# Kernel optimization log

Measured on AMD Instinct MI355X. Metric: run time of the kernel, lower is better.

The kernel has to match this reference:

```python
import jax, jax.numpy as jnp
import numpy as np

N = 50000      # nodes
E = 800000     # edges (before self-loops)
IN_C = 128
H_C = 64
HEADS = 4
OUT_C = 16
NEG_SLOPE = 0.2  # PyG GATConv default


def setup_inputs() -> dict:
    key = jax.random.key(0)
    ks = jax.random.split(key, 11)
    x = jax.random.normal(ks[0], (N, IN_C), dtype=jnp.float32)
    edge_index = jax.random.randint(ks[1], (2, E), 0, N, dtype=jnp.int64)
    def p(k, shape, fan_in):
        return jax.random.normal(k, shape, dtype=jnp.float32) / np.sqrt(fan_in)
    return {
        "x": x,
        "edge_index": edge_index,
        "W1": p(ks[2], (IN_C, HEADS * H_C), IN_C),
        "att_src1": p(ks[3], (HEADS, H_C), H_C),
        "att_dst1": p(ks[4], (HEADS, H_C), H_C),
        "b1": jnp.zeros((HEADS * H_C,), dtype=jnp.float32),
        "W2": p(ks[5], (HEADS * H_C, OUT_C), HEADS * H_C),
        "att_src2": p(ks[6], (1, OUT_C), OUT_C),
        "att_dst2": p(ks[7], (1, OUT_C), OUT_C),
        "b2": jnp.zeros((OUT_C,), dtype=jnp.float32),
    }


def _gat_layer(x, src, dst, W, a_src, a_dst, b, concat):
    n = x.shape[0]
    heads, C = a_src.shape
    h = (x @ W).reshape(n, heads, C)                      # [N,H,C]
    al_s = jnp.einsum('nhc,hc->nh', h, a_src)             # [N,H]
    al_d = jnp.einsum('nhc,hc->nh', h, a_dst)
    e = jax.nn.leaky_relu(al_s[src] + al_d[dst], NEG_SLOPE)  # [E,H]
    # segment softmax over destination neighborhoods
    m = jax.lax.stop_gradient(jax.ops.segment_max(e, dst, num_segments=n))
    p = jnp.exp(e - m[dst])
    denom = jax.ops.segment_sum(p, dst, num_segments=n)
    alpha = p / (denom[dst] + 1e-16)                      # [E,H]
    out = jax.ops.segment_sum(alpha[:, :, None] * h[src], dst, num_segments=n)  # [N,H,C]
    out = out.reshape(n, heads * C) if concat else out.mean(axis=1)
    return out + b


def reference(x, edge_index, W1, att_src1, att_dst1, b1, W2, att_src2, att_dst2, b2):
    # PyG GATConv add_self_loops=True
    loop = jnp.arange(N, dtype=edge_index.dtype)
    src = jnp.concatenate([edge_index[0], loop])
    dst = jnp.concatenate([edge_index[1], loop])
    h = jax.nn.relu(_gat_layer(x, src, dst, W1, att_src1, att_dst1, b1, True))
    out = _gat_layer(h, src, dst, W2, att_src2, att_dst2, b2, False)
    return jax.nn.log_softmax(out, axis=-1)
```

## Files before the change

### kernel.cpp

```cpp
#include <hip/hip_runtime.h>
#include <hip/hip_fp16.h>
#include <cstdint>
#include <cstddef>

#define NEG 0.2f

typedef _Float16 f16x8 __attribute__((ext_vector_type(8)));
typedef float f32x4 __attribute__((ext_vector_type(4)));

__device__ inline float lrelu(float v) { return v > 0.f ? v : NEG * v; }

__global__ void k_swzW(const float* __restrict__ W1, f16x8* __restrict__ W1s) {
  int tau = blockIdx.x * 256 + threadIdx.x;
  if (tau >= 4096) return;
  int l = tau & 63, ct = (tau >> 6) & 15, ks = tau >> 10;
  int col = ct * 16 + (l & 15);
  f16x8 v;
  #pragma unroll
  for (int j = 0; j < 8; j++) {
    int k = ks * 32 + ((j < 4) ? ((l >> 4) * 4 + j) : (16 + (l >> 4) * 4 + (j - 4)));
    v[j] = (_Float16)W1[k * 256 + col];
  }
  W1s[tau] = v;
}

__global__ __launch_bounds__(256) void k_gemm1f(const float* __restrict__ X,
                                                const f16x8* __restrict__ W1s,
                                                const float* __restrict__ as1,
                                                const float* __restrict__ ad1,
                                                __half* __restrict__ H16,
                                                float* __restrict__ als,
                                                float* __restrict__ ald, int N) {
  __shared__ __align__(16) char lds[32768];
  _Float16* A = (_Float16*)lds;
  int t = threadIdx.x;
  int rb = blockIdx.x * 64;
  int l = t & 63, wv = t >> 6;

  #pragma unroll
  for (int i = 0; i < 8; i++) {
    int idx = i * 256 + t;
    int row = idx >> 5, q = idx & 31;
    int gr = rb + row; if (gr >= N) gr = N - 1;
    float4 xv = *(const float4*)(X + (size_t)gr * 128 + q * 4);
    int ks = q >> 3, g = q & 3, hg = (q >> 2) & 1;
    int gran = (ks * 4 + g) ^ (row & 7);
    _Float16* dst = A + row * 128 + gran * 8 + hg * 4;
    dst[0] = (_Float16)xv.x; dst[1] = (_Float16)xv.y;
    dst[2] = (_Float16)xv.z; dst[3] = (_Float16)xv.w;
  }
  __syncthreads();

  f32x4 acc[4][4] = {};
  #pragma unroll
  for (int ks = 0; ks < 4; ks++) {
    f16x8 bfr[4];
    #pragma unroll
    for (int ct = 0; ct < 4; ct++)
      bfr[ct] = W1s[(ks * 16 + wv * 4 + ct) * 64 + l];
    #pragma unroll
    for (int rt = 0; rt < 4; rt++) {
      int row = rt * 16 + (l & 15);
      int gran = (ks * 4 + (l >> 4)) ^ (row & 7);
      f16x8 afr = *(const f16x8*)(A + row * 128 + gran * 8);
      #pragma unroll
      for (int ct = 0; ct < 4; ct++)
        acc[rt][ct] = __builtin_amdgcn_mfma_f32_16x16x32_f16(afr, bfr[ct], acc[rt][ct], 0, 0, 0);
    }
  }

  float asv[4], adv[4];
  #pragma unroll
  for (int ct = 0; ct < 4; ct++) {
    asv[ct] = as1[wv * 64 + ct * 16 + (l & 15)];
    adv[ct] = ad1[wv * 64 + ct * 16 + (l & 15)];
  }
  #pragma unroll
  for (int rt = 0; rt < 4; rt++) {
    #pragma unroll
    for (int j = 0; j < 4; j++) {
      float ps = 0.f, pd = 0.f;
      #pragma unroll
      for (int ct = 0; ct < 4; ct++) {
        ps += acc[rt][ct][j] * asv[ct];
        pd += acc[rt][ct][j] * adv[ct];
      }
      ps += __shfl_xor(ps, 1); ps += __shfl_xor(ps, 2);
      ps += __shfl_xor(ps, 4); ps += __shfl_xor(ps, 8);
      pd += __shfl_xor(pd, 1); pd += __shfl_xor(pd, 2);
      pd += __shfl_xor(pd, 4); pd += __shfl_xor(pd, 8);
      if ((l & 15) == 0) {
        int gr = rb + rt * 16 + (l >> 4) * 4 + j;
        if (gr < N) { als[gr * 4 + wv] = ps; ald[gr * 4 + wv] = pd; }
      }
    }
  }

  __syncthreads();
  _Float16* HL = (_Float16*)lds;
  #pragma unroll
  for (int rt = 0; rt < 4; rt++) {
    #pragma unroll
    for (int j = 0; j < 4; j++) {
      int row = rt * 16 + (l >> 4) * 4 + j;
      #pragma unroll
      for (int ct = 0; ct < 4; ct++) {
        int col = wv * 64 + ct * 16 + (l & 15);
        int g2 = (col >> 3) ^ ((row & 7) << 2);
        HL[row * 256 + g2 * 8 + (col & 7)] = (_Float16)acc[rt][ct][j];
      }
    }
  }
  __syncthreads();
  #pragma unroll
  for (int i = 0; i < 8; i++) {
    int idx = i * 256 + t;
    int row = idx >> 5, g = idx & 31;
    int g2 = g ^ ((row & 7) << 2);
    f32x4 v = *(const f32x4*)(HL + row * 256 + g2 * 8);
    int gr = rb + row;
    if (gr < N) *(f32x4*)((char*)H16 + (size_t)gr * 512 + g * 16) = v;
  }
}

__global__ void k_deg(const int* __restrict__ ei, int* __restrict__ deg, int E, int ET) {
  int e = blockIdx.x * 256 + threadIdx.x;
  if (e >= ET) return;
  int d = (e < E) ? ei[E + e] : e - E;
  atomicAdd(&deg[d], 1);
}

__global__ __launch_bounds__(256) void k_scan_partial(const int* __restrict__ deg,
                                                      int* __restrict__ bsum, int N) {
  __shared__ int sd[256];
  int t = threadIdx.x;
  int base = blockIdx.x * 1024 + t * 4;
  int s = 0;
  #pragma unroll
  for (int j = 0; j < 4; j++) { int i = base + j; s += (i < N) ? deg[i] : 0; }
  sd[t] = s;
  __syncthreads();
  for (int o = 128; o > 0; o >>= 1) {
    if (t < o) sd[t] += sd[t + o];
    __syncthreads();
  }
  if (t == 0) bsum[blockIdx.x] = sd[0];
}

__global__ void k_scan_sums(const int* __restrict__ bsum, int* __restrict__ boff,
                            int* __restrict__ offsets, int NB, int N) {
  if (threadIdx.x == 0 && blockIdx.x == 0) {
    int run = 0;
    for (int i = 0; i < NB; i++) { boff[i] = run; run += bsum[i]; }
    offsets[N] = run;
  }
}

__global__ __launch_bounds__(256) void k_scan_final(const int* __restrict__ deg,
                                                    const int* __restrict__ boff,
                                                    int* __restrict__ offsets,
                                                    int* __restrict__ cursor, int N) {
  __shared__ int sd[256];
  int t = threadIdx.x;
  int base = blockIdx.x * 1024 + t * 4;
  int v[4]; int s = 0;
  #pragma unroll
  for (int j = 0; j < 4; j++) { int i = base + j; v[j] = (i < N) ? deg[i] : 0; s += v[j]; }
  int my = s;
  sd[t] = s;
  __syncthreads();
  for (int o = 1; o < 256; o <<= 1) {
    int add = (t >= o) ? sd[t - o] : 0;
    __syncthreads();
    sd[t] += add;
    __syncthreads();
  }
  int run = sd[t] - my + boff[blockIdx.x];
  #pragma unroll
  for (int j = 0; j < 4; j++) {
    int i = base + j;
    if (i < N) { offsets[i] = run; cursor[i] = run; run += v[j]; }
  }
}

__global__ void k_fill(const int* __restrict__ ei, int* __restrict__ cursor,
                       int* __restrict__ csr_src, int E, int ET) {
  int e = blockIdx.x * 256 + threadIdx.x;
  if (e >= ET) return;
  int s, d;
  if (e < E) { s = ei[e]; d = ei[E + e]; } else { s = d = e - E; }
  int pos = atomicAdd(&cursor[d], 1);
  csr_src[pos] = s;
}

__device__ inline void acc8(float4 v, float p, float* a, float& s) {
  __half2 h0 = __builtin_bit_cast(__half2, v.x);
  __half2 h1 = __builtin_bit_cast(__half2, v.y);
  __half2 h2 = __builtin_bit_cast(__half2, v.z);
  __half2 h3 = __builtin_bit_cast(__half2, v.w);
  float2 f0 = __half22float2(h0), f1 = __half22float2(h1);
  float2 f2 = __half22float2(h2), f3 = __half22float2(h3);
  a[0] += p * f0.x; a[1] += p * f0.y; a[2] += p * f1.x; a[3] += p * f1.y;
  a[4] += p * f2.x; a[5] += p * f2.y; a[6] += p * f3.x; a[7] += p * f3.y;
  s += p;
}

__global__ __launch_bounds__(256) void k_agg1(const int* __restrict__ off,
                                              const int* __restrict__ csr_src,
                                              const float* __restrict__ als1,
                                              const float* __restrict__ ald1,
                                              const float4* __restrict__ H16,
                                              const float* __restrict__ b1,
                                              __half* __restrict__ H2, int N) {
  int t = threadIdx.x;
  int n = blockIdx.x * 8 + (t >> 5);
  if (n >= N) return;
  int lane = t & 31;
  int g = lane >> 3;
  float aldn = ald1[n * 4 + g];
  int st = off[n], en = off[n + 1];
  float a[8] = {0.f, 0.f, 0.f, 0.f, 0.f, 0.f, 0.f, 0.f};
  float s = 0.f;
  int i = st;
  for (; i + 4 <= en; i += 4) {
    int s0 = csr_src[i], s1 = csr_src[i + 1], s2 = csr_src[i + 2], s3 = csr_src[i + 3];
    float p0 = __expf(lrelu(als1[s0 * 4 + g] + aldn));
    float p1 = __expf(lrelu(als1[s1 * 4 + g] + aldn));
    float p2 = __expf(lrelu(als1[s2 * 4 + g] + aldn));
    float p3 = __expf(lrelu(als1[s3 * 4 + g] + aldn));
    float4 v0 = H16[(size_t)s0 * 32 + lane];
    float4 v1 = H16[(size_t)s1 * 32 + lane];
    float4 v2 = H16[(size_t)s2 * 32 + lane];
    float4 v3 = H16[(size_t)s3 * 32 + lane];
    acc8(v0, p0, a, s); acc8(v1, p1, a, s); acc8(v2, p2, a, s); acc8(v3, p3, a, s);
  }
  for (; i < en; i++) {
    int s0 = csr_src[i];
    float p0 = __expf(lrelu(als1[s0 * 4 + g] + aldn));
    float4 v0 = H16[(size_t)s0 * 32 + lane];
    acc8(v0, p0, a, s);
  }
  float inv = 1.f / (s + 1e-16f);
  int c0 = lane * 8;
  float4 bb0 = *(const float4*)(b1 + c0);
  float4 bb1 = *(const float4*)(b1 + c0 + 4);
  f16x8 o;
  o[0] = (_Float16)fmaxf(a[0] * inv + bb0.x, 0.f);
  o[1] = (_Float16)fmaxf(a[1] * inv + bb0.y, 0.f);
  o[2] = (_Float16)fmaxf(a[2] * inv + bb0.z, 0.f);
  o[3] = (_Float16)fmaxf(a[3] * inv + bb0.w, 0.f);
  o[4] = (_Float16)fmaxf(a[4] * inv + bb1.x, 0.f);
  o[5] = (_Float16)fmaxf(a[5] * inv + bb1.y, 0.f);
  o[6] = (_Float16)fmaxf(a[6] * inv + bb1.z, 0.f);
  o[7] = (_Float16)fmaxf(a[7] * inv + bb1.w, 0.f);
  *(f16x8*)((char*)H2 + (size_t)n * 512 + lane * 16) = o;
}

__global__ __launch_bounds__(256) void k_gemm2(const __half* __restrict__ H2,
                                               const float* __restrict__ W2,
                                               const float* __restrict__ as2,
                                               const float* __restrict__ ad2,
                                               float* __restrict__ Z,
                                               float* __restrict__ als2,
                                               float* __restrict__ ald2, int N) {
  __shared__ float w2s[4096];
  int t = threadIdx.x;
  for (int i = t; i < 4096; i += 256) w2s[i] = W2[i];
  __syncthreads();
  int n = blockIdx.x * 16 + (t >> 4);
  int c = t & 15;
  if (n >= N) return;
  const f16x8* hp = (const f16x8*)((const char*)H2 + (size_t)n * 512);
  float acc = 0.f;
  #pragma unroll 8
  for (int kb = 0; kb < 32; kb++) {
    f16x8 hv = hp[kb];
    #pragma unroll
    for (int j = 0; j < 8; j++)
      acc += (float)hv[j] * w2s[(kb * 8 + j) * 16 + c];
  }
  Z[(size_t)n * 16 + c] = acc;
  float ps = acc * as2[c], pd = acc * ad2[c];
  #pragma unroll
  for (int o = 8; o > 0; o >>= 1) {
    ps += __shfl_down(ps, o, 16);
    pd += __shfl_down(pd, o, 16);
  }
  if (c == 0) { als2[n] = ps; ald2[n] = pd; }
}

__global__ __launch_bounds__(256) void k_agg2x(const int* __restrict__ off,
                                               const int* __restrict__ csr_src,
                                               const float* __restrict__ als2,
                                               const float* __restrict__ ald2,
                                               const float* __restrict__ Z,
                                               const float* __restrict__ b2,
                                               float* __restrict__ out, int N) {
  int t = threadIdx.x;
  int n = blockIdx.x * 16 + (t >> 4);
  if (n >= N) return;
  int c = t & 15;
  float aldn = ald2[n];
  int st = off[n], en = off[n + 1];
  float s = 0.f, acc = 0.f;
  int i = st;
  for (; i + 4 <= en; i += 4) {
    int s0 = csr_src[i], s1 = csr_src[i + 1], s2 = csr_src[i + 2], s3 = csr_src[i + 3];
    float p0 = __expf(lrelu(als2[s0] + aldn));
    float p1 = __expf(lrelu(als2[s1] + aldn));
    float p2 = __expf(lrelu(als2[s2] + aldn));
    float p3 = __expf(lrelu(als2[s3] + aldn));
    float z0 = Z[(size_t)s0 * 16 + c];
    float z1 = Z[(size_t)s1 * 16 + c];
    float z2 = Z[(size_t)s2 * 16 + c];
    float z3 = Z[(size_t)s3 * 16 + c];
    acc += p0 * z0 + p1 * z1 + p2 * z2 + p3 * z3;
    s += p0 + p1 + p2 + p3;
  }
  for (; i < en; i++) {
    int s0 = csr_src[i];
    float p0 = __expf(lrelu(als2[s0] + aldn));
    acc += p0 * Z[(size_t)s0 * 16 + c];
    s += p0;
  }
  float v = acc / (s + 1e-16f) + b2[c];
  float mx = v;
  #pragma unroll
  for (int o = 8; o > 0; o >>= 1) mx = fmaxf(mx, __shfl_xor(mx, o, 16));
  float ex = __expf(v - mx);
  float sm = ex;
  #pragma unroll
  for (int o = 8; o > 0; o >>= 1) sm += __shfl_xor(sm, o, 16);
  out[(size_t)n * 16 + c] = v - mx - logf(sm);
}

extern "C" void kernel_launch(void* const* d_in, const int* in_sizes, int n_in,
                              void* d_out, int out_size, void* d_ws, size_t ws_size,
                              hipStream_t stream) {
  const float* x   = (const float*)d_in[0];
  const int*   ei  = (const int*)d_in[1];
  const float* W1  = (const float*)d_in[2];
  const float* as1 = (const float*)d_in[3];
  const float* ad1 = (const float*)d_in[4];
  const float* b1  = (const float*)d_in[5];
  const float* W2  = (const float*)d_in[6];
  const float* as2 = (const float*)d_in[7];
  const float* ad2 = (const float*)d_in[8];
  const float* b2  = (const float*)d_in[9];
  float* out = (float*)d_out;

  int N  = in_sizes[0] / 128;
  int E  = in_sizes[1] / 2;
  int ET = E + N;
  int NB = (N + 1023) / 1024;

  char* w = (char*)d_ws;
  size_t off_b = 0;
  auto alloc = [&](size_t bytes) -> char* {
    size_t start = (off_b + 255) & ~(size_t)255;
    off_b = start + bytes;
    return w + start;
  };
  __half*   h16  = (__half*)alloc((size_t)N * 256 * 2);
  __half*   h2   = (__half*)alloc((size_t)N * 256 * 2);
  f16x8*    w1s  = (f16x8*)alloc((size_t)4096 * 16);
  float*    als1 = (float*)alloc((size_t)N * 4 * 4);
  float*    ald1 = (float*)alloc((size_t)N * 4 * 4);
  int*      deg  = (int*)alloc((size_t)N * 4);
  int*      offs = (int*)alloc((size_t)(N + 1) * 4);
  int*      cur  = (int*)alloc((size_t)N * 4);
  int*      bsum = (int*)alloc((size_t)NB * 4);
  int*      boff = (int*)alloc((size_t)NB * 4);
  int*      csrs = (int*)alloc((size_t)ET * 4);
  float*    z    = (float*)alloc((size_t)N * 16 * 4);
  float*    als2 = (float*)alloc((size_t)N * 4);
  float*    ald2 = (float*)alloc((size_t)N * 4);

  hipMemsetAsync(deg, 0, (size_t)N * 4, stream);

  k_swzW<<<16, 256, 0, stream>>>(W1, w1s);
  k_gemm1f<<<(N + 63) / 64, 256, 0, stream>>>(x, w1s, as1, ad1, h16, als1, ald1, N);
  k_deg<<<(ET + 255) / 256, 256, 0, stream>>>(ei, deg, E, ET);
  k_scan_partial<<<NB, 256, 0, stream>>>(deg, bsum, N);
  k_scan_sums<<<1, 1, 0, stream>>>(bsum, boff, offs, NB, N);
  k_scan_final<<<NB, 256, 0, stream>>>(deg, boff, offs, cur, N);
  k_fill<<<(ET + 255) / 256, 256, 0, stream>>>(ei, cur, csrs, E, ET);
  k_agg1<<<(N + 7) / 8, 256, 0, stream>>>(offs, csrs, als1, ald1, (const float4*)h16, b1, h2, N);
  k_gemm2<<<(N + 15) / 16, 256, 0, stream>>>(h2, W2, as2, ad2, z, als2, ald2, N);
  k_agg2x<<<(N + 15) / 16, 256, 0, stream>>>(offs, csrs, als2, ald2, z, b2, out, N);
}
```

Measured before the change: 242.1 us.

## Split neighbor lists across two thread groups and merge small prep kernels

Both aggregation kernels now give each destination node two thread groups, each walking half of the edge list, and combine the partial sums with a cross-lane shuffle before the epilogue. This doubles the parallelism per node to hide gather latency, at the cost of half the threads idling during the epilogue and more blocks. The W1 swizzle is folded into the degree-count kernel, and the single-thread block-offset scan is removed by having each scan_final block sum the preceding block totals itself. Together these cut the number of kernel launches.

```diff
diff --git a/kernel.cpp b/kernel.cpp
--- a/kernel.cpp
+++ b/kernel.cpp
@@ -10,18 +10,26 @@
 
 __device__ inline float lrelu(float v) { return v > 0.f ? v : NEG * v; }
 
-__global__ void k_swzW(const float* __restrict__ W1, f16x8* __restrict__ W1s) {
-  int tau = blockIdx.x * 256 + threadIdx.x;
-  if (tau >= 4096) return;
-  int l = tau & 63, ct = (tau >> 6) & 15, ks = tau >> 10;
-  int col = ct * 16 + (l & 15);
-  f16x8 v;
-  #pragma unroll
-  for (int j = 0; j < 8; j++) {
-    int k = ks * 32 + ((j < 4) ? ((l >> 4) * 4 + j) : (16 + (l >> 4) * 4 + (j - 4)));
-    v[j] = (_Float16)W1[k * 256 + col];
-  }
-  W1s[tau] = v;
+__global__ void k_pre(const int* __restrict__ ei, int* __restrict__ deg,
+                      const float* __restrict__ W1, f16x8* __restrict__ W1s,
+                      int E, int ET) {
+  int e = blockIdx.x * 256 + threadIdx.x;
+  if (e < ET) {
+    int d = (e < E) ? ei[E + e] : e - E;
+    atomicAdd(&deg[d], 1);
+  }
+  if (blockIdx.x < 16) {
+    int tau = blockIdx.x * 256 + threadIdx.x;
+    int l = tau & 63, ct = (tau >> 6) & 15, ks = tau >> 10;
+    int col = ct * 16 + (l & 15);
+    f16x8 v;
+    #pragma unroll
+    for (int j = 0; j < 8; j++) {
+      int k = ks * 32 + ((j < 4) ? ((l >> 4) * 4 + j) : (16 + (l >> 4) * 4 + (j - 4)));
+      v[j] = (_Float16)W1[k * 256 + col];
+    }
+    W1s[tau] = v;
+  }
 }
 
 __global__ __launch_bounds__(256) void k_gemm1f(const float* __restrict__ X,
@@ -123,13 +131,6 @@
   }
 }
 
-__global__ void k_deg(const int* __restrict__ ei, int* __restrict__ deg, int E, int ET) {
-  int e = blockIdx.x * 256 + threadIdx.x;
-  if (e >= ET) return;
-  int d = (e < E) ? ei[E + e] : e - E;
-  atomicAdd(&deg[d], 1);
-}
-
 __global__ __launch_bounds__(256) void k_scan_partial(const int* __restrict__ deg,
                                                       int* __restrict__ bsum, int N) {
   __shared__ int sd[256];
@@ -147,22 +148,20 @@
   if (t == 0) bsum[blockIdx.x] = sd[0];
 }
 
-__global__ void k_scan_sums(const int* __restrict__ bsum, int* __restrict__ boff,
-                            int* __restrict__ offsets, int NB, int N) {
-  if (threadIdx.x == 0 && blockIdx.x == 0) {
-    int run = 0;
-    for (int i = 0; i < NB; i++) { boff[i] = run; run += bsum[i]; }
-    offsets[N] = run;
-  }
-}
-
 __global__ __launch_bounds__(256) void k_scan_final(const int* __restrict__ deg,
-                                                    const int* __restrict__ boff,
+                                                    const int* __restrict__ bsum,
                                                     int* __restrict__ offsets,
-                                                    int* __restrict__ cursor, int N) {
+                                                    int* __restrict__ cursor,
+                                                    int N, int NB) {
   __shared__ int sd[256];
-  int t = threadIdx.x;
-  int base = blockIdx.x * 1024 + t * 4;
+  __shared__ int boffs;
+  int b = blockIdx.x, t = threadIdx.x;
+  if (t == 0) {
+    int r = 0;
+    for (int i = 0; i < b; i++) r += bsum[i];
+    boffs = r;
+  }
+  int base = b * 1024 + t * 4;
   int v[4]; int s = 0;
   #pragma unroll
   for (int j = 0; j < 4; j++) { int i = base + j; v[j] = (i < N) ? deg[i] : 0; s += v[j]; }
@@ -175,12 +174,13 @@
     sd[t] += add;
     __syncthreads();
   }
-  int run = sd[t] - my + boff[blockIdx.x];
+  int run = sd[t] - my + boffs;
   #pragma unroll
   for (int j = 0; j < 4; j++) {
     int i = base + j;
     if (i < N) { offsets[i] = run; cursor[i] = run; run += v[j]; }
   }
+  if (b == NB - 1 && t == 255) offsets[N] = boffs + sd[255];
 }
 
 __global__ void k_fill(const int* __restrict__ ei, int* __restrict__ cursor,
@@ -213,12 +213,16 @@
                                               const float* __restrict__ b1,
                                               __half* __restrict__ H2, int N) {
   int t = threadIdx.x;
-  int n = blockIdx.x * 8 + (t >> 5);
+  int n = blockIdx.x * 4 + (t >> 6);
   if (n >= N) return;
   int lane = t & 31;
+  int half = (t >> 5) & 1;
   int g = lane >> 3;
   float aldn = ald1[n * 4 + g];
-  int st = off[n], en = off[n + 1];
+  int st0 = off[n], en0 = off[n + 1];
+  int mid = (st0 + en0 + 1) >> 1;
+  int st = half ? mid : st0;
+  int en = half ? en0 : mid;
   float a[8] = {0.f, 0.f, 0.f, 0.f, 0.f, 0.f, 0.f, 0.f};
   float s = 0.f;
   int i = st;
@@ -240,20 +244,25 @@
     float4 v0 = H16[(size_t)s0 * 32 + lane];
     acc8(v0, p0, a, s);
   }
-  float inv = 1.f / (s + 1e-16f);
-  int c0 = lane * 8;
-  float4 bb0 = *(const float4*)(b1 + c0);
-  float4 bb1 = *(const float4*)(b1 + c0 + 4);
-  f16x8 o;
-  o[0] = (_Float16)fmaxf(a[0] * inv + bb0.x, 0.f);
-  o[1] = (_Float16)fmaxf(a[1] * inv + bb0.y, 0.f);
-  o[2] = (_Float16)fmaxf(a[2] * inv + bb0.z, 0.f);
-  o[3] = (_Float16)fmaxf(a[3] * inv + bb0.w, 0.f);
-  o[4] = (_Float16)fmaxf(a[4] * inv + bb1.x, 0.f);
-  o[5] = (_Float16)fmaxf(a[5] * inv + bb1.y, 0.f);
-  o[6] = (_Float16)fmaxf(a[6] * inv + bb1.z, 0.f);
-  o[7] = (_Float16)fmaxf(a[7] * inv + bb1.w, 0.f);
-  *(f16x8*)((char*)H2 + (size_t)n * 512 + lane * 16) = o;
+  #pragma unroll
+  for (int j = 0; j < 8; j++) a[j] += __shfl_xor(a[j], 32);
+  s += __shfl_xor(s, 32);
+  if (half == 0) {
+    float inv = 1.f / (s + 1e-16f);
+    int c0 = lane * 8;
+    float4 bb0 = *(const float4*)(b1 + c0);
+    float4 bb1 = *(const float4*)(b1 + c0 + 4);
+    f16x8 o;
+    o[0] = (_Float16)fmaxf(a[0] * inv + bb0.x, 0.f);
+    o[1] = (_Float16)fmaxf(a[1] * inv + bb0.y, 0.f);
+    o[2] = (_Float16)fmaxf(a[2] * inv + bb0.z, 0.f);
+    o[3] = (_Float16)fmaxf(a[3] * inv + bb0.w, 0.f);
+    o[4] = (_Float16)fmaxf(a[4] * inv + bb1.x, 0.f);
+    o[5] = (_Float16)fmaxf(a[5] * inv + bb1.y, 0.f);
+    o[6] = (_Float16)fmaxf(a[6] * inv + bb1.z, 0.f);
+    o[7] = (_Float16)fmaxf(a[7] * inv + bb1.w, 0.f);
+    *(f16x8*)((char*)H2 + (size_t)n * 512 + lane * 16) = o;
+  }
 }
 
 __global__ __launch_bounds__(256) void k_gemm2(const __half* __restrict__ H2,
@@ -297,11 +306,15 @@
                                                const float* __restrict__ b2,
                                                float* __restrict__ out, int N) {
   int t = threadIdx.x;
-  int n = blockIdx.x * 16 + (t >> 4);
+  int n = blockIdx.x * 8 + (t >> 5);
   if (n >= N) return;
   int c = t & 15;
+  int half = (t >> 4) & 1;
   float aldn = ald2[n];
-  int st = off[n], en = off[n + 1];
+  int st0 = off[n], en0 = off[n + 1];
+  int mid = (st0 + en0 + 1) >> 1;
+  int st = half ? mid : st0;
+  int en = half ? en0 : mid;
   float s = 0.f, acc = 0.f;
   int i = st;
   for (; i + 4 <= en; i += 4) {
@@ -323,15 +336,19 @@
     acc += p0 * Z[(size_t)s0 * 16 + c];
     s += p0;
   }
-  float v = acc / (s + 1e-16f) + b2[c];
-  float mx = v;
-  #pragma unroll
-  for (int o = 8; o > 0; o >>= 1) mx = fmaxf(mx, __shfl_xor(mx, o, 16));
-  float ex = __expf(v - mx);
-  float sm = ex;
-  #pragma unroll
-  for (int o = 8; o > 0; o >>= 1) sm += __shfl_xor(sm, o, 16);
-  out[(size_t)n * 16 + c] = v - mx - logf(sm);
+  acc += __shfl_xor(acc, 16);
+  s += __shfl_xor(s, 16);
+  if (half == 0) {
+    float v = acc / (s + 1e-16f) + b2[c];
+    float mx = v;
+    #pragma unroll
+    for (int o = 8; o > 0; o >>= 1) mx = fmaxf(mx, __shfl_xor(mx, o, 16));
+    float ex = __expf(v - mx);
+    float sm = ex;
+    #pragma unroll
+    for (int o = 8; o > 0; o >>= 1) sm += __shfl_xor(sm, o, 16);
+    out[(size_t)n * 16 + c] = v - mx - logf(sm);
+  }
 }
 
 extern "C" void kernel_launch(void* const* d_in, const int* in_sizes, int n_in,
@@ -370,7 +387,6 @@
   int*      offs = (int*)alloc((size_t)(N + 1) * 4);
   int*      cur  = (int*)alloc((size_t)N * 4);
   int*      bsum = (int*)alloc((size_t)NB * 4);
-  int*      boff = (int*)alloc((size_t)NB * 4);
   int*      csrs = (int*)alloc((size_t)ET * 4);
   float*    z    = (float*)alloc((size_t)N * 16 * 4);
   float*    als2 = (float*)alloc((size_t)N * 4);
@@ -378,14 +394,12 @@
 
   hipMemsetAsync(deg, 0, (size_t)N * 4, stream);
 
-  k_swzW<<<16, 256, 0, stream>>>(W1, w1s);
+  k_pre<<<(ET + 255) / 256, 256, 0, stream>>>(ei, deg, W1, w1s, E, ET);
   k_gemm1f<<<(N + 63) / 64, 256, 0, stream>>>(x, w1s, as1, ad1, h16, als1, ald1, N);
-  k_deg<<<(ET + 255) / 256, 256, 0, stream>>>(ei, deg, E, ET);
   k_scan_partial<<<NB, 256, 0, stream>>>(deg, bsum, N);
-  k_scan_sums<<<1, 1, 0, stream>>>(bsum, boff, offs, NB, N);
-  k_scan_final<<<NB, 256, 0, stream>>>(deg, boff, offs, cur, N);
+  k_scan_final<<<NB, 256, 0, stream>>>(deg, bsum, offs, cur, N, NB);
   k_fill<<<(ET + 255) / 256, 256, 0, stream>>>(ei, cur, csrs, E, ET);
-  k_agg1<<<(N + 7) / 8, 256, 0, stream>>>(offs, csrs, als1, ald1, (const float4*)h16, b1, h2, N);
+  k_agg1<<<(N + 3) / 4, 256, 0, stream>>>(offs, csrs, als1, ald1, (const float4*)h16, b1, h2, N);
   k_gemm2<<<(N + 15) / 16, 256, 0, stream>>>(h2, W2, as2, ad2, z, als2, ald2, N);
-  k_agg2x<<<(N + 15) / 16, 256, 0, stream>>>(offs, csrs, als2, ald2, z, b2, out, N);
-}
+  k_agg2x<<<(N + 7) / 8, 256, 0, stream>>>(offs, csrs, als2, ald2, z, b2, out, N);
+}
```

Result: faster. 233.1 us (median of 2 runs) (-3.7%).
